# Performance work log

Measured on AMD Instinct MI355X. Metric: run time of the kernel, lower is better.

## Reference

```python
import jax, jax.numpy as jnp
import numpy as np

N, C = 16384, 4096
MARGIN = 0.1


def setup_inputs() -> dict:
    key = jax.random.key(0)
    k1, k2 = jax.random.split(key)
    cossim = jax.random.normal(k1, (N, C), dtype=jnp.float32)
    correct = jax.random.randint(k2, (N,), 0, C)
    target = jax.nn.one_hot(correct, C, dtype=jnp.int32)  # one-hot [N, C]
    return {"cossim": cossim, "target": target}


def reference(cossim, target):
    # correct column per row (target is one-hot)
    correct_idx = jnp.argmax(target, axis=1)  # [N]
    correct_sim = jnp.take_along_axis(cossim, correct_idx[:, None], axis=1)  # [N, 1]
    # hinge = clamp(margin + sim - correct_sim, min=0), excluding the correct column
    hinge = jnp.maximum(MARGIN + cossim - correct_sim, 0.0)  # [N, C]
    is_correct = target == 1
    hinge = jnp.where(is_correct, 0.0, hinge)
    loss = jnp.sum(hinge) / N
    return loss
```

## Files before the change

### kernel.cpp

```cpp
#include <hip/hip_runtime.h>

#define N_ROWS 16384
#define N_COLS 4096
#define MARGIN 0.1f
#define BLOCK  256
#define WAVES  4
#define ROWS_PER_WAVE 2
#define NBLK (N_ROWS / (WAVES * ROWS_PER_WAVE))
#define V4_PER_ROW (N_COLS / 4)

typedef float vf4 __attribute__((ext_vector_type(4)));
typedef int   vi4 __attribute__((ext_vector_type(4)));

__global__ __launch_bounds__(BLOCK) void
mm_fused_kernel(const float* __restrict__ cossim,
                const int* __restrict__ target,
                float* __restrict__ partials) {
    const vf4* __restrict__ c4 = (const vf4*)cossim;
    const vi4* __restrict__ t4 = (const vi4*)target;
    const int lane = threadIdx.x & 63, wave = threadIdx.x >> 6;

    vf4 accv = {0.0f, 0.0f, 0.0f, 0.0f};
#pragma unroll
    for (int r = 0; r < ROWS_PER_WAVE; ++r) {
        const unsigned row = (blockIdx.x * WAVES + wave) * ROWS_PER_WAVE + r;
        const size_t rowv4 = (size_t)row * V4_PER_ROW;

        int col = 0;
        for (int i = 0; i < V4_PER_ROW / 128; ++i) {
            const vi4 tA = t4[rowv4 + i * 128 + lane];
            const vi4 tB = t4[rowv4 + i * 128 + 64 + lane];
            const int nzA = tA[0] | tA[1] | tA[2] | tA[3];
            const int nzB = tB[0] | tB[1] | tB[2] | tB[3];
            const unsigned long long m = __ballot((nzA | nzB) != 0);
            if (m) {
                int v4i = i * 128 + lane;
                int e;
                if (nzA) {
                    e = tA[0] ? 0 : tA[1] ? 1 : tA[2] ? 2 : 3;
                } else {
                    v4i += 64;
                    e = tB[0] ? 0 : tB[1] ? 1 : tB[2] ? 2 : 3;
                }
                const int src = (int)__ffsll(m) - 1;
                col = __shfl(v4i * 4 + e, src, 64);
                break;
            }
        }

        const float s_row = cossim[(size_t)row * N_COLS + col];
        const float mc = MARGIN - s_row;

#pragma unroll 8
        for (int k = 0; k < V4_PER_ROW / 64; ++k) {
            const vf4 c = c4[rowv4 + k * 64 + lane];
            accv[0] += fmaxf(mc + c[0], 0.0f);
            accv[1] += fmaxf(mc + c[1], 0.0f);
            accv[2] += fmaxf(mc + c[2], 0.0f);
            accv[3] += fmaxf(mc + c[3], 0.0f);
        }
    }

    float acc = (accv[0] + accv[1]) + (accv[2] + accv[3]);

#pragma unroll
    for (int off = 32; off > 0; off >>= 1)
        acc += __shfl_down(acc, off, 64);
    __shared__ float s_acc[WAVES];
    if (lane == 0) s_acc[wave] = acc;
    __syncthreads();
    if (threadIdx.x == 0)
        partials[blockIdx.x] = s_acc[0] + s_acc[1] + s_acc[2] + s_acc[3];
}

__global__ __launch_bounds__(BLOCK) void
mm_reduce_kernel(const float* __restrict__ partials, float* __restrict__ out) {
    const int t = threadIdx.x;
    float acc = 0.0f;
    for (int i = t; i < NBLK; i += BLOCK) acc += partials[i];
#pragma unroll
    for (int off = 32; off > 0; off >>= 1)
        acc += __shfl_down(acc, off, 64);
    __shared__ float s_wave[BLOCK / 64];
    const int lane = t & 63, wave = t >> 6;
    if (lane == 0) s_wave[wave] = acc;
    __syncthreads();
    if (t == 0)
        out[0] = (s_wave[0] + s_wave[1] + s_wave[2] + s_wave[3]) * (1.0f / N_ROWS)
                 - MARGIN;
}

extern "C" void kernel_launch(void* const* d_in, const int* in_sizes, int n_in,
                              void* d_out, int out_size, void* d_ws, size_t ws_size,
                              hipStream_t stream) {
    const float* cossim = (const float*)d_in[0];
    const int*   target = (const int*)d_in[1];
    float* out      = (float*)d_out;
    float* partials = (float*)d_ws;

    mm_fused_kernel<<<NBLK, BLOCK, 0, stream>>>(cossim, target, partials);
    mm_reduce_kernel<<<1, BLOCK, 0, stream>>>(partials, out);
}
```

Measured before the change: 487.0 us.

## Load full target and cossim rows into registers and extract correct value branchlessly

Each wave now loads its entire target row and cossim row into registers up front (16 vec4 loads each) instead of scanning the target with an early-exit ballot loop and then re-reading cossim. The correct-class similarity is pulled out with bitwise masks and a single ballot/shuffle, removing the serial dependency between the target search and the cossim stream. This raises memory-level parallelism but reads the whole target row where the old loop could stop early, and it costs 128+ extra VGPRs per lane, which may lower occupancy.

```diff
diff --git a/kernel.cpp b/kernel.cpp
--- a/kernel.cpp
+++ b/kernel.cpp
@@ -24,40 +24,38 @@
 #pragma unroll
     for (int r = 0; r < ROWS_PER_WAVE; ++r) {
         const unsigned row = (blockIdx.x * WAVES + wave) * ROWS_PER_WAVE + r;
-        const size_t rowv4 = (size_t)row * V4_PER_ROW;
+        const size_t rowv4 = (size_t)row * V4_PER_ROW + lane;
 
-        int col = 0;
-        for (int i = 0; i < V4_PER_ROW / 128; ++i) {
-            const vi4 tA = t4[rowv4 + i * 128 + lane];
-            const vi4 tB = t4[rowv4 + i * 128 + 64 + lane];
-            const int nzA = tA[0] | tA[1] | tA[2] | tA[3];
-            const int nzB = tB[0] | tB[1] | tB[2] | tB[3];
-            const unsigned long long m = __ballot((nzA | nzB) != 0);
-            if (m) {
-                int v4i = i * 128 + lane;
-                int e;
-                if (nzA) {
-                    e = tA[0] ? 0 : tA[1] ? 1 : tA[2] ? 2 : 3;
-                } else {
-                    v4i += 64;
-                    e = tB[0] ? 0 : tB[1] ? 1 : tB[2] ? 2 : 3;
-                }
-                const int src = (int)__ffsll(m) - 1;
-                col = __shfl(v4i * 4 + e, src, 64);
-                break;
-            }
+        vi4 t[16];
+#pragma unroll
+        for (int k = 0; k < 16; ++k)
+            t[k] = t4[rowv4 + k * 64];
+        vf4 c[16];
+#pragma unroll
+        for (int k = 0; k < 16; ++k)
+            c[k] = c4[rowv4 + k * 64];
+
+        vi4 sv = {0, 0, 0, 0}, nz = {0, 0, 0, 0};
+#pragma unroll
+        for (int k = 0; k < 16; ++k) {
+            const vi4 cb  = __builtin_bit_cast(vi4, c[k]);
+            const vi4 msk = -t[k];
+            sv |= cb & msk;
+            nz |= t[k];
         }
-
-        const float s_row = cossim[(size_t)row * N_COLS + col];
+        const int lanenz = (nz[0] | nz[1]) | (nz[2] | nz[3]);
+        const unsigned long long m = __ballot(lanenz != 0);
+        const int sb = (sv[0] | sv[1]) | (sv[2] | sv[3]);
+        const float sval  = __builtin_bit_cast(float, sb);
+        const float s_row = __shfl(sval, (int)__ffsll(m) - 1, 64);
         const float mc = MARGIN - s_row;
 
-#pragma unroll 8
-        for (int k = 0; k < V4_PER_ROW / 64; ++k) {
-            const vf4 c = c4[rowv4 + k * 64 + lane];
-            accv[0] += fmaxf(mc + c[0], 0.0f);
-            accv[1] += fmaxf(mc + c[1], 0.0f);
-            accv[2] += fmaxf(mc + c[2], 0.0f);
-            accv[3] += fmaxf(mc + c[3], 0.0f);
+#pragma unroll
+        for (int k = 0; k < 16; ++k) {
+            accv[0] += fmaxf(mc + c[k][0], 0.0f);
+            accv[1] += fmaxf(mc + c[k][1], 0.0f);
+            accv[2] += fmaxf(mc + c[k][2], 0.0f);
+            accv[3] += fmaxf(mc + c[k][3], 0.0f);
         }
     }
 
```

Measured after the change: 492.2 us. About the same (+1.1%).
